# Optimization experiments

Hardware: AMD Instinct MI355X
Metric: run time of the kernel (lower is better)

The kernel has to match this reference:

```python
import jax, jax.numpy as jnp
import numpy as np

N_MODES = 64


def setup_inputs() -> dict:
    key = jax.random.key(0)
    k1, k2, k3 = jax.random.split(key, 3)
    B, Cin, S = 32, 128, 8192
    H, Hc, M = 4, 32, N_MODES  # n_heads, head_channels, n_modes (Cout = H*Hc = 128)
    x = jax.random.normal(k1, (B, Cin, S), dtype=jnp.float32)
    # per-head init scale: std = 0.01 * 2**h (matches _init_weights)
    scale = (0.01 * 2.0 ** jnp.arange(H, dtype=jnp.float32)).reshape(H, 1, 1, 1)
    w_real = jax.random.normal(k2, (H, Cin, Hc, M), dtype=jnp.float32) * scale
    w_imag = jax.random.normal(k3, (H, Cin, Hc, M), dtype=jnp.float32) * scale
    return {"x": x, "w_real": w_real, "w_imag": w_imag}


def reference(x, w_real, w_imag):
    B, Cin, S = x.shape
    H, _, Hc, M = w_real.shape
    Cout = H * Hc
    x_ft = jnp.fft.rfft(x, axis=-1)                 # [B, Cin, F] complex64
    F = x_ft.shape[-1]
    M = min(M, F)                                    # static
    w = (w_real + 1j * w_imag).astype(x_ft.dtype)    # [H, Cin, Hc, M]
    # fused batched complex contraction over all heads/modes at once
    out = jnp.einsum('bim,hiom->bhom', x_ft[:, :, :M], w[..., :M])  # [B, H, Hc, M]
    out = out.reshape(B, Cout, M)                    # head h -> channels [h*Hc, (h+1)*Hc)
    out_ft = jnp.zeros((B, Cout, F), dtype=x_ft.dtype).at[:, :, :M].set(out)
    return jnp.fft.irfft(out_ft, n=S, axis=-1)       # [B, Cout, S] float32
```

## Files before the change

kernel.cpp:

```cpp
#include <hip/hip_runtime.h>
#include <cstdio>

#define S_LEN 8192
#define NM 64

typedef short s8v __attribute__((ext_vector_type(8)));
typedef float f4  __attribute__((ext_vector_type(4)));
typedef _Float16 h8 __attribute__((ext_vector_type(8)));
typedef _Float16 h4v __attribute__((ext_vector_type(4)));

static __device__ inline unsigned short f2bf(float f) {
    unsigned int u = __builtin_bit_cast(unsigned int, f);
    u = (u + 0x7FFFu + ((u >> 16) & 1u)) >> 16;
    return (unsigned short)u;
}
static __device__ inline float bf2f(unsigned short h) {
    unsigned int u = ((unsigned int)h) << 16;
    return __builtin_bit_cast(float, u);
}

#define SW32(r, k) (((r) * 32) + ((k) ^ ((((r) >> 1) & 3) << 3)))

static __device__ __forceinline__ void glds16(const void* g, void* l) {
    __builtin_amdgcn_global_load_lds(
        (const __attribute__((address_space(1))) unsigned int*)g,
        (__attribute__((address_space(3))) unsigned int*)l, 16, 0, 0);
}

__global__ __launch_bounds__(256) void gen_t1_img(short* __restrict__ Th,
                                                  short* __restrict__ Tl) {
    int tid = blockIdx.x * 256 + threadIdx.x;
    int tile = tid >> 12;
    int sb = tile >> 2, kc = tile & 3;
    int us = tid & 4095;
    int ls = us >> 5, kx = us & 31;
    int lk = kx ^ (((ls >> 1) & 3) << 3);
    int s = sb * 128 + ls;
    int k = kc * 32 + lk;
    int m = k >> 1;
    int p = (m * s) & (S_LEN - 1);
    float ang = (float)p * (6.28318530717958647692f / (float)S_LEN);
    float sn, cs; sincosf(ang, &sn, &cs);
    float v = (k & 1) ? -sn : cs;
    unsigned short h = f2bf(v);
    Th[tid] = (short)h;
    Tl[tid] = (short)f2bf(v - bf2f(h));
}

__global__ __launch_bounds__(256) void gen_b_img(_Float16* __restrict__ Bimg) {
    int tid = blockIdx.x * 256 + threadIdx.x;
    int e = tid & 7;
    int lane = (tid >> 3) & 63;
    int cf = (tid >> 9) & 7;
    int w32 = tid >> 12;
    int rl = lane & 15, kq = lane >> 4;
    int col = cf * 16 + rl;
    int m = col >> 1;
    int k = w32 * 32 + kq * 8 + e;
    int p = (m * k) & (S_LEN - 1);
    float ang = (float)p * (6.28318530717958647692f / (float)S_LEN);
    float sn, cs; sincosf(ang, &sn, &cs);
    Bimg[tid] = (_Float16)((col & 1) ? -sn : cs);
}

#define NSTEP 32
__global__ __launch_bounds__(512, 4) void dft_fwd_mfma(const float* __restrict__ x,
        const _Float16* __restrict__ Bimg, float* __restrict__ P) {
    __shared__ _Float16 abh[2][16 * 128], abl[2][16 * 128];
    const int t = threadIdx.x;
    const int lane = t & 63, w = t >> 6;
    const int rl = lane & 15, kq = lane >> 4;
    const int row0 = blockIdx.x * 16;
    const int ks = blockIdx.y;
    const int rA = t >> 5, cA = (t & 31) * 4;
    const size_t xrow = (size_t)(row0 + rA) * S_LEN + (size_t)ks * (S_LEN / 2) + cA;
    const int usA = rA * 128 + ((((cA >> 3) ^ rA) & 15) << 3) + (cA & 7);
    const size_t bbase = (size_t)ks * 1048576 + (size_t)w * 1024 + (size_t)lane * 16;

    f4 acc = (f4){0.f, 0.f, 0.f, 0.f};
    f4 a0, a1, a2;

    #define LA(SC, AV) AV = *(const f4*)&x[xrow + (size_t)(SC) * 128];

    #define CV(AV, NXT) { h4v hv, lv;                                              \
        _Pragma("unroll")                                                          \
        for (int e = 0; e < 4; ++e) {                                              \
            float f = AV[e]; _Float16 hh = (_Float16)f;                            \
            hv[e] = hh; lv[e] = (_Float16)(f - (float)hh);                         \
        }                                                                          \
        *(h4v*)&abh[NXT][usA] = hv;                                                \
        *(h4v*)&abl[NXT][usA] = lv; }

    #define MM(CUR, SC) {                                                          \
        h8 Bf0 = *(const h8*)((const char*)Bimg + bbase + (size_t)((SC)*4+0)*8192);\
        h8 Bf1 = *(const h8*)((const char*)Bimg + bbase + (size_t)((SC)*4+1)*8192);\
        h8 Bf2 = *(const h8*)((const char*)Bimg + bbase + (size_t)((SC)*4+2)*8192);\
        h8 Bf3 = *(const h8*)((const char*)Bimg + bbase + (size_t)((SC)*4+3)*8192);\
        _Pragma("unroll")                                                          \
        for (int wd = 0; wd < 4; ++wd) {                                           \
            const int sl = ((((wd << 2) + kq) ^ rl) & 15) << 3;                    \
            h8 Ah = *(const h8*)&abh[CUR][rl * 128 + sl];                          \
            h8 Al = *(const h8*)&abl[CUR][rl * 128 + sl];                          \
            h8 Bf = (wd == 0) ? Bf0 : (wd == 1) ? Bf1 : (wd == 2) ? Bf2 : Bf3;     \
            acc = __builtin_amdgcn_mfma_f32_16x16x32_f16(Ah, Bf, acc, 0, 0, 0);    \
            acc = __builtin_amdgcn_mfma_f32_16x16x32_f16(Al, Bf, acc, 0, 0, 0);    \
        } }

    #define BAR  __builtin_amdgcn_sched_barrier(0);                                \
        asm volatile("s_waitcnt lgkmcnt(0)" ::: "memory");                         \
        __builtin_amdgcn_sched_barrier(0);                                         \
        __builtin_amdgcn_s_barrier();                                              \
        __builtin_amdgcn_sched_barrier(0);

    #define STEP(SC, LAC, AVL, AVC, NXT, CUR)                                      \
        LA(LAC, AVL); CV(AVC, NXT); MM(CUR, SC); BAR

    LA(0, a0); LA(1, a1); LA(2, a2);
    CV(a0, 0);
    BAR
    for (int s = 0; s < 24; s += 6) {
        STEP(s + 0, s + 3, a0, a1, 1, 0)
        STEP(s + 1, s + 4, a1, a2, 0, 1)
        STEP(s + 2, s + 5, a2, a0, 1, 0)
        STEP(s + 3, s + 6, a0, a1, 0, 1)
        STEP(s + 4, s + 7, a1, a2, 1, 0)
        STEP(s + 5, s + 8, a2, a0, 0, 1)
    }
    STEP(24, 27, a0, a1, 1, 0)
    STEP(25, 28, a1, a2, 0, 1)
    STEP(26, 29, a2, a0, 1, 0)
    STEP(27, 30, a0, a1, 0, 1)
    STEP(28, 31, a1, a2, 1, 0)
    STEP(29, 31, a2, a0, 0, 1)
    CV(a1, 1); MM(0, 30); BAR
    MM(1, 31);

    float* Pks = P + (size_t)ks * 4096 * 128;
    #pragma unroll
    for (int r = 0; r < 4; ++r)
        Pks[(size_t)(row0 + kq * 4 + r) * 128 + w * 16 + rl] = acc[r];
}

__global__ __launch_bounds__(256) void ksum(const float* __restrict__ P,
                                            float* __restrict__ X) {
    int i = (blockIdx.x * 256 + threadIdx.x) * 4;
    f4 s = *(const f4*)&P[i];
    s += *(const f4*)&P[524288 + i];
    *(f4*)&X[i] = s;
}

__global__ __launch_bounds__(256) void mode_contract(const float* __restrict__ X,
        const float* __restrict__ w_real, const float* __restrict__ w_imag,
        short* __restrict__ C2h, short* __restrict__ C2l) {
    __shared__ float xr[32][128], xi[32][128];
    __shared__ float wr[128][32], wi[128][32];
    const int m = blockIdx.x, h = blockIdx.y, t = threadIdx.x;
    #pragma unroll
    for (int it = 0; it < 16; ++it) {
        int li = t + it * 256;
        int b = li >> 7, i = li & 127;
        const float2 v = *(const float2*)&X[(size_t)(b * 128 + i) * 128 + 2 * m];
        xr[b][i] = v.x; xi[b][i] = v.y;
        int i2 = li >> 5, o = li & 31;
        size_t off = ((size_t)((h * 128 + i2) * 32 + o)) * NM + m;
        wr[i2][o] = w_real[off];
        wi[i2][o] = w_imag[off];
    }
    __syncthreads();
    const int o = t & 31;
    const int b0 = (t >> 5) * 4;
    float re[4] = {0.f, 0.f, 0.f, 0.f}, im[4] = {0.f, 0.f, 0.f, 0.f};
    for (int i = 0; i < 128; ++i) {
        float wrv = wr[i][o], wiv = wi[i][o];
        #pragma unroll
        for (int j = 0; j < 4; ++j) {
            float a = xr[b0 + j][i], c = xi[b0 + j][i];
            re[j] += a * wrv - c * wiv;
            im[j] += a * wiv + c * wrv;
        }
    }
    const float alpha = (m == 0) ? (1.0f / (float)S_LEN) : (2.0f / (float)S_LEN);
    const int kc = m >> 4;
    const int lk = (2 * m) & 31;
    #pragma unroll
    for (int j = 0; j < 4; ++j) {
        int row = (b0 + j) * 128 + h * 32 + o;
        float vr = alpha * re[j], vi = alpha * im[j];
        unsigned short hr = f2bf(vr), hi_ = f2bf(vi);
        float lr = vr - bf2f(hr), li_ = vi - bf2f(hi_);
        int rb = row >> 7, lr_ = row & 127;
        size_t ui = ((size_t)(rb * 4 + kc) * 4096 + SW32(lr_, lk)) >> 1;
        ((unsigned int*)C2h)[ui] = ((unsigned int)hi_ << 16) | hr;
        ((unsigned int*)C2l)[ui] = ((unsigned int)f2bf(li_) << 16) | f2bf(lr);
    }
}

__global__ __launch_bounds__(256, 2) void idft_mfma(const short* __restrict__ C2h,
        const short* __restrict__ C2l, const short* __restrict__ T1h,
        const short* __restrict__ T1l, float* __restrict__ y) {
    __shared__ short ah[2][4096], al[2][4096];
    __shared__ short bh[2][4096], bl[2][4096];
    const int t = threadIdx.x;
    const int lane = t & 63, wid = t >> 6;
    const int wm = (wid >> 1) * 64, wn = (wid & 1) * 64;
    const int sb = blockIdx.x;
    const int rb = blockIdx.y;
    f4 acc[4][4];
    #pragma unroll
    for (int i = 0; i < 4; ++i)
        #pragma unroll
        for (int j = 0; j < 4; ++j) acc[i][j] = (f4){0.f, 0.f, 0.f, 0.f};

    #define DMA3(kc, buf)  {                                                       \
        const size_t ta = (size_t)(rb * 4 + (kc)) * 8192;                          \
        const size_t tb = (size_t)(sb * 4 + (kc)) * 8192;                          \
        const int wo = wid * 2048 + lane * 16;                                     \
        glds16((const char*)C2h + ta + wo,        (char*)&ah[buf][0] + wid * 2048);        \
        glds16((const char*)C2h + ta + wo + 1024, (char*)&ah[buf][0] + wid * 2048 + 1024); \
        glds16((const char*)C2l + ta + wo,        (char*)&al[buf][0] + wid * 2048);        \
        glds16((const char*)C2l + ta + wo + 1024, (char*)&al[buf][0] + wid * 2048 + 1024); \
        glds16((const char*)T1h + tb + wo,        (char*)&bh[buf][0] + wid * 2048);        \
        glds16((const char*)T1h + tb + wo + 1024, (char*)&bh[buf][0] + wid * 2048 + 1024); \
        glds16((const char*)T1l + tb + wo,        (char*)&bl[buf][0] + wid * 2048);        \
        glds16((const char*)T1l + tb + wo + 1024, (char*)&bl[buf][0] + wid * 2048 + 1024); }

    DMA3(0, 0);
    __syncthreads();
    #pragma unroll
    for (int kc = 0; kc < 4; ++kc) {
        const int cur = kc & 1;
        if (kc < 3) DMA3(kc + 1, cur ^ 1);
        {
            const int kk = (lane >> 4) * 8, rl = lane & 15;
            s8v Ah[4], Al[4], Bh[4], Bl[4];
            #pragma unroll
            for (int mf = 0; mf < 4; ++mf) {
                int us = SW32(wm + mf * 16 + rl, kk);
                Ah[mf] = *(const s8v*)&ah[cur][us];
                Al[mf] = *(const s8v*)&al[cur][us];
            }
            #pragma unroll
            for (int nf = 0; nf < 4; ++nf) {
                int us = SW32(wn + nf * 16 + rl, kk);
                Bh[nf] = *(const s8v*)&bh[cur][us];
                Bl[nf] = *(const s8v*)&bl[cur][us];
            }
            #pragma unroll
            for (int mf = 0; mf < 4; ++mf)
                #pragma unroll
                for (int nf = 0; nf < 4; ++nf)
                    acc[mf][nf] = __builtin_amdgcn_mfma_f32_16x16x32_bf16(Ah[mf], Bh[nf], acc[mf][nf], 0, 0, 0);
            #pragma unroll
            for (int mf = 0; mf < 4; ++mf)
                #pragma unroll
                for (int nf = 0; nf < 4; ++nf)
                    acc[mf][nf] = __builtin_amdgcn_mfma_f32_16x16x32_bf16(Al[mf], Bh[nf], acc[mf][nf], 0, 0, 0);
            #pragma unroll
            for (int mf = 0; mf < 4; ++mf)
                #pragma unroll
                for (int nf = 0; nf < 4; ++nf)
                    acc[mf][nf] = __builtin_amdgcn_mfma_f32_16x16x32_bf16(Ah[mf], Bl[nf], acc[mf][nf], 0, 0, 0);
        }
        __syncthreads();
    }
    #pragma unroll
    for (int mf = 0; mf < 4; ++mf) {
        int rr = rb * 128 + wm + mf * 16 + (lane >> 4) * 4;
        #pragma unroll
        for (int nf = 0; nf < 4; ++nf) {
            int c = sb * 128 + wn + nf * 16 + (lane & 15);
            #pragma unroll
            for (int r = 0; r < 4; ++r)
                __builtin_nontemporal_store(acc[mf][nf][r], &y[(size_t)(rr + r) * S_LEN + c]);
        }
    }
}

extern "C" void kernel_launch(void* const* d_in, const int* in_sizes, int n_in,
                              void* d_out, int out_size, void* d_ws, size_t ws_size,
                              hipStream_t stream) {
    const float* x      = (const float*)d_in[0];
    const float* w_real = (const float*)d_in[1];
    const float* w_imag = (const float*)d_in[2];
    float* y = (float*)d_out;

    const size_t TBL = (size_t)S_LEN * 128;
    char* w0 = (char*)d_ws;
    short* T1h     = (short*)w0;
    short* T1l     = T1h + TBL;
    _Float16* Bimg = (_Float16*)(T1l + TBL);
    float* X       = (float*)(Bimg + TBL);
    short* C2h     = (short*)(X + (size_t)4096 * 128);
    short* C2l     = C2h + (size_t)4096 * 128;
    float* P       = (float*)(C2l + (size_t)4096 * 128);
    const size_t TOTAL = (size_t)((char*)(P + 2 * (size_t)4096 * 128) - w0);
    if (ws_size < TOTAL) {
        fprintf(stderr, "kernel_launch: ws too small (%zu < %zu bytes)\n", ws_size, TOTAL);
        return;
    }

    gen_t1_img<<<(S_LEN * 128) / 256, 256, 0, stream>>>(T1h, T1l);
    gen_b_img<<<(S_LEN * 128) / 256, 256, 0, stream>>>(Bimg);
    dft_fwd_mfma<<<dim3(4096 / 16, 2), 512, 0, stream>>>(x, Bimg, P);
    ksum<<<512, 256, 0, stream>>>(P, X);
    mode_contract<<<dim3(NM, 4), 256, 0, stream>>>(X, w_real, w_imag, C2h, C2l);
    idft_mfma<<<dim3(S_LEN / 128, 4096 / 128), 256, 0, stream>>>(C2h, C2l, T1h, T1l, y);
}
```

Baseline: 129.9 us.

## Retile forward DFT GEMM with LDS-staged twiddles, 8-way K split, cosine lookup table

```diff
diff --git a/kernel.cpp b/kernel.cpp
--- a/kernel.cpp
+++ b/kernel.cpp
@@ -7,7 +7,6 @@
 typedef short s8v __attribute__((ext_vector_type(8)));
 typedef float f4  __attribute__((ext_vector_type(4)));
 typedef _Float16 h8 __attribute__((ext_vector_type(8)));
-typedef _Float16 h4v __attribute__((ext_vector_type(4)));
 
 static __device__ inline unsigned short f2bf(float f) {
     unsigned int u = __builtin_bit_cast(unsigned int, f);
@@ -27,7 +26,13 @@
         (__attribute__((address_space(3))) unsigned int*)l, 16, 0, 0);
 }
 
-__global__ __launch_bounds__(256) void gen_t1_img(short* __restrict__ Th,
+__global__ __launch_bounds__(256) void gen_master(float* __restrict__ tab) {
+    int p = blockIdx.x * 256 + threadIdx.x;
+    tab[p] = cosf((float)p * (6.28318530717958647692f / (float)S_LEN));
+}
+
+__global__ __launch_bounds__(256) void gen_t1_img(const float* __restrict__ tab,
+                                                  short* __restrict__ Th,
                                                   short* __restrict__ Tl) {
     int tid = blockIdx.x * 256 + threadIdx.x;
     int tile = tid >> 12;
@@ -38,114 +43,140 @@
     int s = sb * 128 + ls;
     int k = kc * 32 + lk;
     int m = k >> 1;
-    int p = (m * s) & (S_LEN - 1);
-    float ang = (float)p * (6.28318530717958647692f / (float)S_LEN);
-    float sn, cs; sincosf(ang, &sn, &cs);
-    float v = (k & 1) ? -sn : cs;
+    int p = (m * s + ((k & 1) << 11)) & (S_LEN - 1);
+    float v = tab[p];
     unsigned short h = f2bf(v);
     Th[tid] = (short)h;
     Tl[tid] = (short)f2bf(v - bf2f(h));
 }
 
-__global__ __launch_bounds__(256) void gen_b_img(_Float16* __restrict__ Bimg) {
+__global__ __launch_bounds__(256) void gen_b_img(const float* __restrict__ tab,
+                                                 _Float16* __restrict__ Bimg) {
     int tid = blockIdx.x * 256 + threadIdx.x;
-    int e = tid & 7;
-    int lane = (tid >> 3) & 63;
-    int cf = (tid >> 9) & 7;
-    int w32 = tid >> 12;
-    int rl = lane & 15, kq = lane >> 4;
-    int col = cf * 16 + rl;
-    int m = col >> 1;
-    int k = w32 * 32 + kq * 8 + e;
-    int p = (m * k) & (S_LEN - 1);
-    float ang = (float)p * (6.28318530717958647692f / (float)S_LEN);
-    float sn, cs; sincosf(ang, &sn, &cs);
-    Bimg[tid] = (_Float16)((col & 1) ? -sn : cs);
-}
-
-#define NSTEP 32
+    int tk = tid >> 13;
+    int us = tid & 8191;
+    int c = us >> 6;
+    int wl = us & 63;
+    int slot = wl >> 3, e = wl & 7;
+    int k = ((slot ^ (c & 7)) << 3) | e;
+    int kg = tk * 64 + k;
+    int m = c >> 1;
+    int p = (m * kg + ((c & 1) << 11)) & (S_LEN - 1);
+    Bimg[tid] = (_Float16)tab[p];
+}
+
 __global__ __launch_bounds__(512, 4) void dft_fwd_mfma(const float* __restrict__ x,
         const _Float16* __restrict__ Bimg, float* __restrict__ P) {
-    __shared__ _Float16 abh[2][16 * 128], abl[2][16 * 128];
+    __shared__ _Float16 abh[2][4096], abl[2][4096];
+    __shared__ _Float16 bb[2][8192];
     const int t = threadIdx.x;
     const int lane = t & 63, w = t >> 6;
     const int rl = lane & 15, kq = lane >> 4;
-    const int row0 = blockIdx.x * 16;
+    const int wr = w >> 2, wc = w & 3;
+    const int row0 = blockIdx.x * 64;
     const int ks = blockIdx.y;
-    const int rA = t >> 5, cA = (t & 31) * 4;
-    const size_t xrow = (size_t)(row0 + rA) * S_LEN + (size_t)ks * (S_LEN / 2) + cA;
-    const int usA = rA * 128 + ((((cA >> 3) ^ rA) & 15) << 3) + (cA & 7);
-    const size_t bbase = (size_t)ks * 1048576 + (size_t)w * 1024 + (size_t)lane * 16;
-
-    f4 acc = (f4){0.f, 0.f, 0.f, 0.f};
-    f4 a0, a1, a2;
-
-    #define LA(SC, AV) AV = *(const f4*)&x[xrow + (size_t)(SC) * 128];
-
-    #define CV(AV, NXT) { h4v hv, lv;                                              \
+    const int rA = t >> 3, sA = t & 7;
+    const size_t xrow = (size_t)(row0 + rA) * S_LEN + (size_t)ks * 1024 + (size_t)sA * 8;
+    const int usA = rA * 64 + ((sA ^ (rA & 7)) << 3);
+    const size_t bby = (size_t)ks * 16 * 16384 + (size_t)t * 32;
+
+    f4 acc[2][2];
+    #pragma unroll
+    for (int i = 0; i < 2; ++i)
+        #pragma unroll
+        for (int j = 0; j < 2; ++j) acc[i][j] = (f4){0.f, 0.f, 0.f, 0.f};
+
+    f4 aA0, aA1, aB0, aB1;
+    h8 bA0, bA1, bB0, bB1;
+
+    #define LA(SC, A0, A1) { A0 = *(const f4*)&x[xrow + (size_t)(SC) * 64];        \
+                             A1 = *(const f4*)&x[xrow + (size_t)(SC) * 64 + 4]; }
+    #define LB(SC, B0, B1) { const char* g = (const char*)Bimg + bby +             \
+                                 (size_t)(SC) * 16384;                             \
+                             B0 = *(const h8*)g; B1 = *(const h8*)(g + 16); }
+    #define CV(A0, A1, NXT) { h8 hv, lv;                                           \
         _Pragma("unroll")                                                          \
         for (int e = 0; e < 4; ++e) {                                              \
-            float f = AV[e]; _Float16 hh = (_Float16)f;                            \
+            float f = A0[e]; _Float16 hh = (_Float16)f;                            \
             hv[e] = hh; lv[e] = (_Float16)(f - (float)hh);                         \
         }                                                                          \
-        *(h4v*)&abh[NXT][usA] = hv;                                                \
-        *(h4v*)&abl[NXT][usA] = lv; }
-
-    #define MM(CUR, SC) {                                                          \
-        h8 Bf0 = *(const h8*)((const char*)Bimg + bbase + (size_t)((SC)*4+0)*8192);\
-        h8 Bf1 = *(const h8*)((const char*)Bimg + bbase + (size_t)((SC)*4+1)*8192);\
-        h8 Bf2 = *(const h8*)((const char*)Bimg + bbase + (size_t)((SC)*4+2)*8192);\
-        h8 Bf3 = *(const h8*)((const char*)Bimg + bbase + (size_t)((SC)*4+3)*8192);\
         _Pragma("unroll")                                                          \
-        for (int wd = 0; wd < 4; ++wd) {                                           \
-            const int sl = ((((wd << 2) + kq) ^ rl) & 15) << 3;                    \
-            h8 Ah = *(const h8*)&abh[CUR][rl * 128 + sl];                          \
-            h8 Al = *(const h8*)&abl[CUR][rl * 128 + sl];                          \
-            h8 Bf = (wd == 0) ? Bf0 : (wd == 1) ? Bf1 : (wd == 2) ? Bf2 : Bf3;     \
-            acc = __builtin_amdgcn_mfma_f32_16x16x32_f16(Ah, Bf, acc, 0, 0, 0);    \
-            acc = __builtin_amdgcn_mfma_f32_16x16x32_f16(Al, Bf, acc, 0, 0, 0);    \
+        for (int e = 0; e < 4; ++e) {                                              \
+            float f = A1[e]; _Float16 hh = (_Float16)f;                            \
+            hv[4 + e] = hh; lv[4 + e] = (_Float16)(f - (float)hh);                 \
+        }                                                                          \
+        *(h8*)&abh[NXT][usA] = hv;                                                 \
+        *(h8*)&abl[NXT][usA] = lv; }
+    #define WB(B0, B1, NXT) { *(h8*)&bb[NXT][t * 16] = B0;                         \
+                              *(h8*)&bb[NXT][t * 16 + 8] = B1; }
+    #define MM(CUR) { _Pragma("unroll")                                            \
+        for (int ksl = 0; ksl < 2; ++ksl) {                                        \
+            const int sb_ = ksl * 4 + kq;                                          \
+            h8 Ah0, Al0, Ah1, Al1, Bv0, Bv1;                                       \
+            { int r = wr * 32 + rl;      int u = r * 64 + ((sb_ ^ (r & 7)) << 3);  \
+              Ah0 = *(const h8*)&abh[CUR][u]; Al0 = *(const h8*)&abl[CUR][u]; }    \
+            { int r = wr * 32 + 16 + rl; int u = r * 64 + ((sb_ ^ (r & 7)) << 3);  \
+              Ah1 = *(const h8*)&abh[CUR][u]; Al1 = *(const h8*)&abl[CUR][u]; }    \
+            { int c = wc * 32 + rl;      int u = c * 64 + ((sb_ ^ (c & 7)) << 3);  \
+              Bv0 = *(const h8*)&bb[CUR][u]; }                                     \
+            { int c = wc * 32 + 16 + rl; int u = c * 64 + ((sb_ ^ (c & 7)) << 3);  \
+              Bv1 = *(const h8*)&bb[CUR][u]; }                                     \
+            acc[0][0] = __builtin_amdgcn_mfma_f32_16x16x32_f16(Ah0, Bv0, acc[0][0], 0, 0, 0); \
+            acc[0][1] = __builtin_amdgcn_mfma_f32_16x16x32_f16(Ah0, Bv1, acc[0][1], 0, 0, 0); \
+            acc[1][0] = __builtin_amdgcn_mfma_f32_16x16x32_f16(Ah1, Bv0, acc[1][0], 0, 0, 0); \
+            acc[1][1] = __builtin_amdgcn_mfma_f32_16x16x32_f16(Ah1, Bv1, acc[1][1], 0, 0, 0); \
+            acc[0][0] = __builtin_amdgcn_mfma_f32_16x16x32_f16(Al0, Bv0, acc[0][0], 0, 0, 0); \
+            acc[0][1] = __builtin_amdgcn_mfma_f32_16x16x32_f16(Al0, Bv1, acc[0][1], 0, 0, 0); \
+            acc[1][0] = __builtin_amdgcn_mfma_f32_16x16x32_f16(Al1, Bv0, acc[1][0], 0, 0, 0); \
+            acc[1][1] = __builtin_amdgcn_mfma_f32_16x16x32_f16(Al1, Bv1, acc[1][1], 0, 0, 0); \
         } }
-
     #define BAR  __builtin_amdgcn_sched_barrier(0);                                \
         asm volatile("s_waitcnt lgkmcnt(0)" ::: "memory");                         \
         __builtin_amdgcn_sched_barrier(0);                                         \
         __builtin_amdgcn_s_barrier();                                              \
         __builtin_amdgcn_sched_barrier(0);
 
-    #define STEP(SC, LAC, AVL, AVC, NXT, CUR)                                      \
-        LA(LAC, AVL); CV(AVC, NXT); MM(CUR, SC); BAR
-
-    LA(0, a0); LA(1, a1); LA(2, a2);
-    CV(a0, 0);
+    LA(0, aA0, aA1) LA(1, aB0, aB1) LB(0, bA0, bA1) LB(1, bB0, bB1)
+    __builtin_amdgcn_sched_barrier(0);
+    CV(aA0, aA1, 0) WB(bA0, bA1, 0)
     BAR
-    for (int s = 0; s < 24; s += 6) {
-        STEP(s + 0, s + 3, a0, a1, 1, 0)
-        STEP(s + 1, s + 4, a1, a2, 0, 1)
-        STEP(s + 2, s + 5, a2, a0, 1, 0)
-        STEP(s + 3, s + 6, a0, a1, 0, 1)
-        STEP(s + 4, s + 7, a1, a2, 1, 0)
-        STEP(s + 5, s + 8, a2, a0, 0, 1)
-    }
-    STEP(24, 27, a0, a1, 1, 0)
-    STEP(25, 28, a1, a2, 0, 1)
-    STEP(26, 29, a2, a0, 1, 0)
-    STEP(27, 30, a0, a1, 0, 1)
-    STEP(28, 31, a1, a2, 1, 0)
-    STEP(29, 31, a2, a0, 0, 1)
-    CV(a1, 1); MM(0, 30); BAR
-    MM(1, 31);
-
-    float* Pks = P + (size_t)ks * 4096 * 128;
-    #pragma unroll
-    for (int r = 0; r < 4; ++r)
-        Pks[(size_t)(row0 + kq * 4 + r) * 128 + w * 16 + rl] = acc[r];
+    for (int s = 0; s < 14; s += 2) {
+        LA(s + 2, aA0, aA1) LB(s + 2, bA0, bA1)
+        __builtin_amdgcn_sched_barrier(0);
+        CV(aB0, aB1, 1) WB(bB0, bB1, 1)
+        MM(0)
+        BAR
+        LA(s + 3, aB0, aB1) LB(s + 3, bB0, bB1)
+        __builtin_amdgcn_sched_barrier(0);
+        CV(aA0, aA1, 0) WB(bA0, bA1, 0)
+        MM(1)
+        BAR
+    }
+    LA(15, aA0, aA1) LB(15, bA0, bA1)
+    __builtin_amdgcn_sched_barrier(0);
+    CV(aB0, aB1, 1) WB(bB0, bB1, 1)
+    MM(0)
+    BAR
+    MM(1)
+
+    float* Pks = P + (size_t)ks * 524288;
+    #pragma unroll
+    for (int mf = 0; mf < 2; ++mf)
+        #pragma unroll
+        for (int nf = 0; nf < 2; ++nf)
+            #pragma unroll
+            for (int r = 0; r < 4; ++r)
+                Pks[(size_t)(row0 + wr * 32 + mf * 16 + kq * 4 + r) * 128
+                    + wc * 32 + nf * 16 + rl] = acc[mf][nf][r];
 }
 
 __global__ __launch_bounds__(256) void ksum(const float* __restrict__ P,
                                             float* __restrict__ X) {
     int i = (blockIdx.x * 256 + threadIdx.x) * 4;
-    f4 s = *(const f4*)&P[i];
-    s += *(const f4*)&P[524288 + i];
+    f4 s = (f4){0.f, 0.f, 0.f, 0.f};
+    #pragma unroll
+    for (int ks = 0; ks < 8; ++ks)
+        s += *(const f4*)&P[(size_t)ks * 524288 + i];
     *(f4*)&X[i] = s;
 }
 
@@ -290,18 +321,20 @@
     short* T1l     = T1h + TBL;
     _Float16* Bimg = (_Float16*)(T1l + TBL);
     float* X       = (float*)(Bimg + TBL);
-    short* C2h     = (short*)(X + (size_t)4096 * 128);
-    short* C2l     = C2h + (size_t)4096 * 128;
-    float* P       = (float*)(C2l + (size_t)4096 * 128);
-    const size_t TOTAL = (size_t)((char*)(P + 2 * (size_t)4096 * 128) - w0);
+    float* tab     = X + (size_t)4096 * 128;
+    float* P       = tab + S_LEN;
+    short* C2h     = (short*)P;
+    short* C2l     = C2h + TBL;
+    const size_t TOTAL = (size_t)((char*)(P + 8 * (size_t)4096 * 128) - w0);
     if (ws_size < TOTAL) {
         fprintf(stderr, "kernel_launch: ws too small (%zu < %zu bytes)\n", ws_size, TOTAL);
         return;
     }
 
-    gen_t1_img<<<(S_LEN * 128) / 256, 256, 0, stream>>>(T1h, T1l);
-    gen_b_img<<<(S_LEN * 128) / 256, 256, 0, stream>>>(Bimg);
-    dft_fwd_mfma<<<dim3(4096 / 16, 2), 512, 0, stream>>>(x, Bimg, P);
+    gen_master<<<S_LEN / 256, 256, 0, stream>>>(tab);
+    gen_t1_img<<<(S_LEN * 128) / 256, 256, 0, stream>>>(tab, T1h, T1l);
+    gen_b_img<<<(S_LEN * 128) / 256, 256, 0, stream>>>(tab, Bimg);
+    dft_fwd_mfma<<<dim3(64, 8), 512, 0, stream>>>(x, Bimg, P);
     ksum<<<512, 256, 0, stream>>>(P, X);
     mode_contract<<<dim3(NM, 4), 256, 0, stream>>>(X, w_real, w_imag, C2h, C2l);
     idft_mfma<<<dim3(S_LEN / 128, 4096 / 128), 256, 0, stream>>>(C2h, C2l, T1h, T1l, y);
```

Measured after the change: 123.3 us. -5.1%, faster.
